# Kernel optimization log

Measured on AMD Instinct MI355X. Metric: run time of the kernel, lower is better.

The kernel has to match this reference:

```python
import jax, jax.numpy as jnp
import numpy as np

N, E, D, H, A, L = 100000, 600000, 128, 4, 32, 2
C = D // H  # per-head channels


def setup_inputs() -> dict:
    key = jax.random.key(0)
    ks = jax.random.split(key, 16)
    s = 1.0 / np.sqrt(D)
    return {
        "x": jax.random.normal(ks[0], (N, D), jnp.float32),
        "edge_index": jax.random.randint(ks[1], (2, E), 0, N, jnp.int32),
        "edge_attr": jax.random.normal(ks[2], (E, A), jnp.float32),
        # GATv2 params per layer (lin_l: source, lin_r: target, lin_edge: no bias)
        "W_l": jax.random.normal(ks[3], (L, D, D), jnp.float32) * s,
        "b_l": jnp.zeros((L, D), jnp.float32),
        "W_r": jax.random.normal(ks[4], (L, D, D), jnp.float32) * s,
        "b_r": jnp.zeros((L, D), jnp.float32),
        "W_e": jax.random.normal(ks[5], (L, A, D), jnp.float32) * (1.0 / np.sqrt(A)),
        "att": jax.random.normal(ks[6], (L, H, C), jnp.float32) * (1.0 / np.sqrt(C)),
        "bias_out": jnp.zeros((L, D), jnp.float32),
        # residual MLP: Linear -> LayerNorm -> GELU
        "lin_W": jax.random.normal(ks[7], (L, D, D), jnp.float32) * s,
        "lin_b": jnp.zeros((L, D), jnp.float32),
        "ln_gamma": jnp.ones((L, D), jnp.float32),
        "ln_beta": jnp.zeros((L, D), jnp.float32),
    }


def _gatv2_layer(x, src, dst, edge_attr, W_l, b_l, W_r, b_r, W_e, att, bias_out):
    xl = (x @ W_l + b_l).reshape(N, H, C)  # source transform
    xr = (x @ W_r + b_r).reshape(N, H, C)  # target transform
    ea = (edge_attr @ W_e).reshape(E, H, C)
    # GATv2 attention: leaky_relu(x_i + x_j + e), score with att vector
    m = jax.nn.leaky_relu(xl[src] + xr[dst] + ea, negative_slope=0.2)  # [E,H,C]
    logits = jnp.einsum('ehc,hc->eh', m, att)  # [E,H]
    # segment softmax over destination nodes
    mx = jax.ops.segment_max(logits, dst, num_segments=N)  # [N,H]
    ex = jnp.exp(logits - mx[dst])
    denom = jax.ops.segment_sum(ex, dst, num_segments=N)
    alpha = ex / denom[dst]  # [E,H]
    out = jax.ops.segment_sum(xl[src] * alpha[:, :, None], dst, num_segments=N)
    return out.reshape(N, D) + bias_out


def _mlp(h, W, b, gamma, beta):
    h = h @ W + b
    mu = jnp.mean(h, axis=-1, keepdims=True)
    var = jnp.var(h, axis=-1, keepdims=True)
    h = (h - mu) * jax.lax.rsqrt(var + 1e-5) * gamma + beta
    return jax.nn.gelu(h, approximate=False)


def reference(x, edge_index, edge_attr, W_l, b_l, W_r, b_r, W_e, att, bias_out,
              lin_W, lin_b, ln_gamma, ln_beta):
    src, dst = edge_index[0], edge_index[1]
    for i in range(L):
        x_o = _gatv2_layer(x, src, dst, edge_attr,
                           W_l[i], b_l[i], W_r[i], b_r[i], W_e[i], att[i], bias_out[i])
        x_o = _mlp(x_o, lin_W[i], lin_b[i], ln_gamma[i], ln_beta[i])
        x = x + x_o
    return x
```

## Files before the change

### kernel.cpp

```cpp
#include <hip/hip_runtime.h>
#include <cmath>

#define NN 100000
#define EE 600000
#define DD 128
#define HH 4
#define AA 32
#define CC 32
#define LL 2
#define NB ((NN + 255) / 256)
#define GEMM_GRID ((NN + 127) / 128)

typedef unsigned short u16;
typedef unsigned int u32;
typedef __attribute__((ext_vector_type(8))) short bf16x8;
typedef __attribute__((ext_vector_type(4))) float f32x4;

#define MFMA(a, b, c) __builtin_amdgcn_mfma_f32_16x16x32_bf16(a, b, c, 0, 0, 0)

__global__ __launch_bounds__(256) void k_count(const int* __restrict__ ei,
                                               int* __restrict__ cnt) {
  int e = blockIdx.x * 256 + threadIdx.x;
  if (e < EE) atomicAdd(&cnt[ei[EE + e]], 1);
}

__global__ __launch_bounds__(256) void k_scan1(const int* __restrict__ cnt,
                                               int* __restrict__ row_ptr,
                                               int* __restrict__ bsum) {
  __shared__ int buf[256];
  int b = blockIdx.x, t = threadIdx.x;
  int i = b * 256 + t;
  int v = (i < NN) ? cnt[i] : 0;
  buf[t] = v;
  __syncthreads();
  for (int off = 1; off < 256; off <<= 1) {
    int u = (t >= off) ? buf[t - off] : 0;
    __syncthreads();
    buf[t] += u;
    __syncthreads();
  }
  if (i < NN) row_ptr[i] = buf[t] - v;
  if (t == 255) bsum[b] = buf[255];
}

__global__ __launch_bounds__(512) void k_scan2(const int* __restrict__ bsum,
                                               int* __restrict__ boff) {
  __shared__ int buf[512];
  int t = threadIdx.x;
  int v = (t < NB) ? bsum[t] : 0;
  buf[t] = v;
  __syncthreads();
  for (int off = 1; off < 512; off <<= 1) {
    int u = (t >= off) ? buf[t - off] : 0;
    __syncthreads();
    buf[t] += u;
    __syncthreads();
  }
  if (t < NB) boff[t] = buf[t] - v;
}

__global__ __launch_bounds__(256) void k_scan3(int* __restrict__ row_ptr,
                                               const int* __restrict__ boff,
                                               int* __restrict__ cursor) {
  int b = blockIdx.x, t = threadIdx.x;
  int i = b * 256 + t;
  if (i < NN) {
    int v = row_ptr[i] + boff[b];
    row_ptr[i] = v;
    cursor[i] = v;
  }
  if (i == 0) row_ptr[NN] = EE;
}

__global__ __launch_bounds__(256) void k_fill(const int* __restrict__ ei,
                                              int* __restrict__ cursor,
                                              int* __restrict__ csr_e,
                                              int* __restrict__ csr_src) {
  int e = blockIdx.x * 256 + threadIdx.x;
  if (e < EE) {
    int d = ei[EE + e];
    int p = atomicAdd(&cursor[d], 1);
    csr_e[p] = e;
    csr_src[p] = ei[e];
  }
}

__global__ __launch_bounds__(256) void k_wprep(const float* __restrict__ Wl,
                                               const float* __restrict__ Wr,
                                               const float* __restrict__ Wlin,
                                               u16* __restrict__ wth,
                                               u16* __restrict__ wtl) {
  int b = blockIdx.x;
  int m = b >> 6;
  int layer = m / 3, type = m % 3;
  const float* src =
      (type == 0 ? Wl : type == 1 ? Wr : Wlin) + (size_t)layer * DD * DD;
  u16* dh = wth + (size_t)m * DD * DD;
  u16* dl = wtl + (size_t)m * DD * DD;
  int i = (b & 63) * 256 + threadIdx.x;
  int k = i >> 7, n = i & 127;
  float x = src[i];
  u32 u = __float_as_uint(x);
  u32 hr = (u + 0x7FFFu + ((u >> 16) & 1u)) & 0xFFFF0000u;
  float hf = __uint_as_float(hr);
  float d = x - hf;
  u32 u2 = __float_as_uint(d);
  u32 lr = (u2 + 0x7FFFu + ((u2 >> 16) & 1u)) & 0xFFFF0000u;
  dh[n * DD + k] = (u16)(hr >> 16);
  dl[n * DD + k] = (u16)(lr >> 16);
}

__device__ inline void cvt8(const float4& p0, const float4& p1, bf16x8& hi,
                            bf16x8& lo) {
  union { bf16x8 v; u32 u[4]; } H, L;
  float f[8] = {p0.x, p0.y, p0.z, p0.w, p1.x, p1.y, p1.z, p1.w};
#pragma unroll
  for (int i = 0; i < 4; ++i) {
    u32 u0 = __float_as_uint(f[2 * i]), u1 = __float_as_uint(f[2 * i + 1]);
    u32 h0 = u0 & 0xFFFF0000u, h1 = u1 & 0xFFFF0000u;
    H.u[i] = (h0 >> 16) | h1;
    float r0 = f[2 * i] - __uint_as_float(h0);
    float r1 = f[2 * i + 1] - __uint_as_float(h1);
    u32 l0 = __float_as_uint(r0) & 0xFFFF0000u;
    u32 l1 = __float_as_uint(r1) & 0xFFFF0000u;
    L.u[i] = (l0 >> 16) | l1;
  }
  hi = H.v;
  lo = L.v;
}

__device__ inline void load_a(const float* __restrict__ X, long row0, int wid,
                              int q, int ln, bf16x8 ah[2][4], bf16x8 al[2][4]) {
#pragma unroll
  for (int mt = 0; mt < 2; ++mt) {
    long r = row0 + wid * 32 + mt * 16 + ln;
    if (r > NN - 1) r = NN - 1;
    const float* xp = X + r * DD;
#pragma unroll
    for (int ks = 0; ks < 4; ++ks) {
      float4 p0 = *(const float4*)&xp[ks * 32 + q * 8];
      float4 p1 = *(const float4*)&xp[ks * 32 + q * 8 + 4];
      cvt8(p0, p1, ah[mt][ks], al[mt][ks]);
    }
  }
}

__device__ inline void stage_w(const u16* __restrict__ gWh,
                               const u16* __restrict__ gWl, u16* sWh, u16* sWl,
                               int t) {
  const uint4* gh = (const uint4*)gWh;
  const uint4* gl = (const uint4*)gWl;
#pragma unroll
  for (int i = 0; i < 8; ++i) {
    int c = t + 256 * i;
    int row = c >> 4;
    int bo = (c & 15) * 16;
    int dst = row * 256 + (bo ^ ((row & 7) << 4));
    *(uint4*)((char*)sWh + dst) = gh[c];
    *(uint4*)((char*)sWl + dst) = gl[c];
  }
}

__device__ inline void mfma_compute(const u16* sWh, const u16* sWl,
                                    bf16x8 ah[2][4], bf16x8 al[2][4],
                                    f32x4 acc[2][8], int q, int ln) {
#pragma unroll
  for (int ks = 0; ks < 4; ++ks) {
    int base = ks * 64 + q * 16;
#pragma unroll
    for (int nt = 0; nt < 8; ++nt) {
      int nrow = nt * 16 + ln;
      int off = nrow * 256 + (base ^ ((nrow & 7) << 4));
      bf16x8 bh = *(const bf16x8*)((const char*)sWh + off);
      bf16x8 bl = *(const bf16x8*)((const char*)sWl + off);
#pragma unroll
      for (int mt = 0; mt < 2; ++mt) {
        acc[mt][nt] = MFMA(ah[mt][ks], bh, acc[mt][nt]);
        acc[mt][nt] = MFMA(al[mt][ks], bh, acc[mt][nt]);
        acc[mt][nt] = MFMA(ah[mt][ks], bl, acc[mt][nt]);
      }
    }
  }
}

__global__ __launch_bounds__(256, 2) void k_gemm2(
    const float* __restrict__ X, const u16* __restrict__ Wh0,
    const u16* __restrict__ Wl0, const float* __restrict__ b0,
    const u16* __restrict__ Wh1, const u16* __restrict__ Wl1,
    const float* __restrict__ b1, float* __restrict__ O0,
    float* __restrict__ O1) {
  __shared__ u16 sWh[DD * DD];
  __shared__ u16 sWl[DD * DD];
  int t = threadIdx.x, wid = t >> 6, lane = t & 63;
  int q = lane >> 4, ln = lane & 15;
  long row0 = (long)blockIdx.x * 128;

  bf16x8 ah[2][4], al[2][4];
  load_a(X, row0, wid, q, ln, ah, al);

#pragma unroll 1
  for (int rep = 0; rep < 2; ++rep) {
    if (rep) __syncthreads();
    stage_w(rep ? Wh1 : Wh0, rep ? Wl1 : Wl0, sWh, sWl, t);
    __syncthreads();

    f32x4 acc[2][8];
    f32x4 zero = {0.f, 0.f, 0.f, 0.f};
#pragma unroll
    for (int mt = 0; mt < 2; ++mt)
#pragma unroll
      for (int nt = 0; nt < 8; ++nt) acc[mt][nt] = zero;

    mfma_compute(sWh, sWl, ah, al, acc, q, ln);

    const float* bias = rep ? b1 : b0;
    float* Out = rep ? O1 : O0;
    float bv[8];
#pragma unroll
    for (int nt = 0; nt < 8; ++nt) bv[nt] = bias[nt * 16 + ln];
#pragma unroll
    for (int mt = 0; mt < 2; ++mt)
#pragma unroll
      for (int nt = 0; nt < 8; ++nt)
#pragma unroll
        for (int rg = 0; rg < 4; ++rg) {
          long r = row0 + wid * 32 + mt * 16 + 4 * q + rg;
          if (r < NN) Out[r * DD + nt * 16 + ln] = acc[mt][nt][rg] + bv[nt];
        }
  }
}

__global__ __launch_bounds__(256, 2) void k_gemm_epi(
    const float* __restrict__ X, const u16* __restrict__ Wh,
    const u16* __restrict__ Wl, const float* __restrict__ bias,
    float* __restrict__ Out, const float* __restrict__ gamma,
    const float* __restrict__ beta) {
  __shared__ u16 sWh[DD * DD];
  __shared__ u16 sWl[DD * DD];
  int t = threadIdx.x, wid = t >> 6, lane = t & 63;
  int q = lane >> 4, ln = lane & 15;
  long row0 = (long)blockIdx.x * 128;

  bf16x8 ah[2][4], al[2][4];
  load_a(X, row0, wid, q, ln, ah, al);
  stage_w(Wh, Wl, sWh, sWl, t);
  __syncthreads();

  f32x4 acc[2][8];
  f32x4 zero = {0.f, 0.f, 0.f, 0.f};
#pragma unroll
  for (int mt = 0; mt < 2; ++mt)
#pragma unroll
    for (int nt = 0; nt < 8; ++nt) acc[mt][nt] = zero;

  mfma_compute(sWh, sWl, ah, al, acc, q, ln);

  float bv[8], gv[8], bev[8];
#pragma unroll
  for (int nt = 0; nt < 8; ++nt) {
    int c = nt * 16 + ln;
    bv[nt] = bias[c];
    gv[nt] = gamma[c];
    bev[nt] = beta[c];
  }

#pragma unroll
  for (int mt = 0; mt < 2; ++mt) {
    float s[4] = {0.f, 0.f, 0.f, 0.f}, ss[4] = {0.f, 0.f, 0.f, 0.f};
#pragma unroll
    for (int nt = 0; nt < 8; ++nt)
#pragma unroll
      for (int rg = 0; rg < 4; ++rg) {
        float v = acc[mt][nt][rg] + bv[nt];
        acc[mt][nt][rg] = v;
        s[rg] += v;
        ss[rg] += v * v;
      }
#pragma unroll
    for (int rg = 0; rg < 4; ++rg) {
#pragma unroll
      for (int m = 1; m < 16; m <<= 1) {
        s[rg] += __shfl_xor(s[rg], m);
        ss[rg] += __shfl_xor(ss[rg], m);
      }
    }
    float mean[4], inv[4];
#pragma unroll
    for (int rg = 0; rg < 4; ++rg) {
      mean[rg] = s[rg] * (1.f / DD);
      float var = ss[rg] * (1.f / DD) - mean[rg] * mean[rg];
      inv[rg] = rsqrtf(var + 1e-5f);
    }
    const float is2 = 0.70710678118654752440f;
#pragma unroll
    for (int nt = 0; nt < 8; ++nt)
#pragma unroll
      for (int rg = 0; rg < 4; ++rg) {
        long r = row0 + wid * 32 + mt * 16 + 4 * q + rg;
        if (r < NN) {
          int c = nt * 16 + ln;
          float u = (acc[mt][nt][rg] - mean[rg]) * inv[rg] * gv[nt] + bev[nt];
          float res = Out[r * DD + c];
          Out[r * DD + c] = res + 0.5f * u * (1.f + erff(u * is2));
        }
      }
  }
}

__global__ __launch_bounds__(256) void k_attn(const int* __restrict__ row_ptr,
                                              const int* __restrict__ csr_e,
                                              const int* __restrict__ csr_src,
                                              const float* __restrict__ eattr,
                                              const float* __restrict__ We,
                                              const float* __restrict__ att,
                                              const float* __restrict__ xl,
                                              const float* __restrict__ xr,
                                              const float* __restrict__ bias_out,
                                              float* __restrict__ xo) {
  int t = threadIdx.x;
  int wid = t >> 6, l = t & 63;
  int n = blockIdx.x * 4 + wid;
  int ch = 2 * l;

  float2 wreg[32];
#pragma unroll
  for (int a = 0; a < 32; ++a) wreg[a] = *(const float2*)&We[a * DD + ch];
  float2 av = *(const float2*)&att[ch];
  float2 xrv = *(const float2*)&xr[(size_t)n * DD + ch];

  float m = -INFINITY, d = 0.f;
  float ax = 0.f, ay = 0.f;

  int b = row_ptr[n], e2 = row_ptr[n + 1];
#pragma unroll 1
  for (int j = b; j < e2; ++j) {
    int e = __builtin_amdgcn_readfirstlane(csr_e[j]);
    int s = __builtin_amdgcn_readfirstlane(csr_src[j]);

    float eax = 0.f, eay = 0.f;
    const float4* ev = (const float4*)(eattr + (size_t)e * AA);
#pragma unroll
    for (int qq = 0; qq < 8; ++qq) {
      float4 v = ev[qq];
      float2 w0 = wreg[4 * qq + 0], w1 = wreg[4 * qq + 1];
      float2 w2 = wreg[4 * qq + 2], w3 = wreg[4 * qq + 3];
      eax = fmaf(v.x, w0.x, fmaf(v.y, w1.x, fmaf(v.z, w2.x, fmaf(v.w, w3.x, eax))));
      eay = fmaf(v.x, w0.y, fmaf(v.y, w1.y, fmaf(v.z, w2.y, fmaf(v.w, w3.y, eay))));
    }
    float2 xlv = *(const float2*)&xl[(size_t)s * DD + ch];
    float mx = xlv.x + xrv.x + eax;
    float my = xlv.y + xrv.y + eay;
    mx = mx > 0.f ? mx : 0.2f * mx;
    my = my > 0.f ? my : 0.2f * my;
    float lg = av.x * mx + av.y * my;
    lg += __shfl_xor(lg, 1);
    lg += __shfl_xor(lg, 2);
    lg += __shfl_xor(lg, 4);
    lg += __shfl_xor(lg, 8);

    float mn = fmaxf(m, lg);
    float sc = __expf(m - mn);
    float w = __expf(lg - mn);
    d = d * sc + w;
    ax = fmaf(ax, sc, w * xlv.x);
    ay = fmaf(ay, sc, w * xlv.y);
    m = mn;
  }

  float inv = d > 0.f ? 1.f / d : 0.f;
  float2 bo = *(const float2*)&bias_out[ch];
  float2 o = {fmaf(ax, inv, bo.x), fmaf(ay, inv, bo.y)};
  *(float2*)&xo[(size_t)n * DD + ch] = o;
}

extern "C" void kernel_launch(void* const* d_in, const int* in_sizes, int n_in,
                              void* d_out, int out_size, void* d_ws,
                              size_t ws_size, hipStream_t stream) {
  const float* x_in = (const float*)d_in[0];
  const int* ei = (const int*)d_in[1];
  const float* eattr = (const float*)d_in[2];
  const float* W_l = (const float*)d_in[3];
  const float* b_l = (const float*)d_in[4];
  const float* W_r = (const float*)d_in[5];
  const float* b_r = (const float*)d_in[6];
  const float* W_e = (const float*)d_in[7];
  const float* att = (const float*)d_in[8];
  const float* bias_out = (const float*)d_in[9];
  const float* lin_W = (const float*)d_in[10];
  const float* lin_b = (const float*)d_in[11];
  const float* ln_g = (const float*)d_in[12];
  const float* ln_b2 = (const float*)d_in[13];

  float* x = (float*)d_out;

  char* base = (char*)d_ws;
  size_t off = 0;
  auto alloc = [&](size_t bytes) {
    size_t o = off;
    off = (off + bytes + 255) & ~(size_t)255;
    return o;
  };
  float* xl = (float*)(base + alloc((size_t)NN * DD * 4));
  float* xr = (float*)(base + alloc((size_t)NN * DD * 4));
  float* xo = (float*)(base + alloc((size_t)NN * DD * 4));
  int* cnt = (int*)(base + alloc((size_t)NN * 4));
  int* row_ptr = (int*)(base + alloc((size_t)(NN + 1) * 4));
  int* cursor = (int*)(base + alloc((size_t)NN * 4));
  int* bsum = (int*)(base + alloc((size_t)NB * 4));
  int* boff = (int*)(base + alloc((size_t)NB * 4));
  int* csr_e = (int*)(base + alloc((size_t)EE * 4));
  int* csr_src = (int*)(base + alloc((size_t)EE * 4));
  u16* wth = (u16*)(base + alloc((size_t)6 * DD * DD * 2));
  u16* wtl = (u16*)(base + alloc((size_t)6 * DD * DD * 2));

  hipMemcpyAsync(x, x_in, (size_t)NN * DD * 4, hipMemcpyDeviceToDevice, stream);

  k_wprep<<<6 * 64, 256, 0, stream>>>(W_l, W_r, lin_W, wth, wtl);

  hipMemsetAsync(cnt, 0, (size_t)NN * 4, stream);
  k_count<<<(EE + 255) / 256, 256, 0, stream>>>(ei, cnt);
  k_scan1<<<NB, 256, 0, stream>>>(cnt, row_ptr, bsum);
  k_scan2<<<1, 512, 0, stream>>>(bsum, boff);
  k_scan3<<<NB, 256, 0, stream>>>(row_ptr, boff, cursor);
  k_fill<<<(EE + 255) / 256, 256, 0, stream>>>(ei, cursor, csr_e, csr_src);

  for (int i = 0; i < LL; ++i) {
    const u16* h_l = wth + (size_t)(i * 3 + 0) * DD * DD;
    const u16* l_l = wtl + (size_t)(i * 3 + 0) * DD * DD;
    const u16* h_r = wth + (size_t)(i * 3 + 1) * DD * DD;
    const u16* l_r = wtl + (size_t)(i * 3 + 1) * DD * DD;
    const u16* h_e = wth + (size_t)(i * 3 + 2) * DD * DD;
    const u16* l_e = wtl + (size_t)(i * 3 + 2) * DD * DD;
    const float* bl_i = b_l + (size_t)i * DD;
    const float* br_i = b_r + (size_t)i * DD;
    const float* We_i = W_e + (size_t)i * AA * DD;
    const float* att_i = att + (size_t)i * HH * CC;
    const float* bo_i = bias_out + (size_t)i * DD;
    const float* lb_i = lin_b + (size_t)i * DD;
    const float* g_i = ln_g + (size_t)i * DD;
    const float* be_i = ln_b2 + (size_t)i * DD;

    k_gemm2<<<GEMM_GRID, 256, 0, stream>>>(x, h_l, l_l, bl_i, h_r, l_r, br_i,
                                           xl, xr);
    k_attn<<<NN / 4, 256, 0, stream>>>(row_ptr, csr_e, csr_src, eattr, We_i,
                                       att_i, xl, xr, bo_i, xo);
    k_gemm_epi<<<GEMM_GRID, 256, 0, stream>>>(xo, h_e, l_e, lb_i, x, g_i, be_i);
  }
}
```

Before: 898.0 us.

## Permute edge attributes into CSR order and prefetch source rows in attention

The fill kernel now copies each edge's attribute row into destination-sorted CSR order, so the attention kernel streams edge attributes contiguously instead of gathering them through csr_e. The attention loop software-prefetches xl rows two edges ahead, sets a launch-bounds occupancy hint, and splits the edge-feature dot product into explicit FMA chains. The initial device-to-device copy of x is dropped by reading the input directly in layer 0 and passing a separate residual pointer to the epilogue GEMM. The cost is an extra 77 MB permuted attribute buffer written once, in exchange for fewer scattered reads across the two layers.

```diff
diff --git a/kernel.cpp b/kernel.cpp
--- a/kernel.cpp
+++ b/kernel.cpp
@@ -74,14 +74,18 @@
 
 __global__ __launch_bounds__(256) void k_fill(const int* __restrict__ ei,
                                               int* __restrict__ cursor,
-                                              int* __restrict__ csr_e,
-                                              int* __restrict__ csr_src) {
+                                              int* __restrict__ csr_src,
+                                              float* __restrict__ ea_perm,
+                                              const float* __restrict__ eattr) {
   int e = blockIdx.x * 256 + threadIdx.x;
   if (e < EE) {
     int d = ei[EE + e];
     int p = atomicAdd(&cursor[d], 1);
-    csr_e[p] = e;
     csr_src[p] = ei[e];
+    const float4* srow = (const float4*)(eattr + (size_t)e * AA);
+    float4* drow = (float4*)(ea_perm + (size_t)p * AA);
+#pragma unroll
+    for (int i = 0; i < 8; ++i) drow[i] = srow[i];
   }
 }
 
@@ -233,8 +237,8 @@
 __global__ __launch_bounds__(256, 2) void k_gemm_epi(
     const float* __restrict__ X, const u16* __restrict__ Wh,
     const u16* __restrict__ Wl, const float* __restrict__ bias,
-    float* __restrict__ Out, const float* __restrict__ gamma,
-    const float* __restrict__ beta) {
+    const float* __restrict__ resid, float* __restrict__ Out,
+    const float* __restrict__ gamma, const float* __restrict__ beta) {
   __shared__ u16 sWh[DD * DD];
   __shared__ u16 sWl[DD * DD];
   int t = threadIdx.x, wid = t >> 6, lane = t & 63;
@@ -300,23 +304,19 @@
         if (r < NN) {
           int c = nt * 16 + ln;
           float u = (acc[mt][nt][rg] - mean[rg]) * inv[rg] * gv[nt] + bev[nt];
-          float res = Out[r * DD + c];
+          float res = resid[r * DD + c];
           Out[r * DD + c] = res + 0.5f * u * (1.f + erff(u * is2));
         }
       }
   }
 }
 
-__global__ __launch_bounds__(256) void k_attn(const int* __restrict__ row_ptr,
-                                              const int* __restrict__ csr_e,
-                                              const int* __restrict__ csr_src,
-                                              const float* __restrict__ eattr,
-                                              const float* __restrict__ We,
-                                              const float* __restrict__ att,
-                                              const float* __restrict__ xl,
-                                              const float* __restrict__ xr,
-                                              const float* __restrict__ bias_out,
-                                              float* __restrict__ xo) {
+__global__ __launch_bounds__(256, 4) void k_attn(
+    const int* __restrict__ row_ptr, const int* __restrict__ csr_src,
+    const float* __restrict__ ea, const float* __restrict__ We,
+    const float* __restrict__ att, const float* __restrict__ xl,
+    const float* __restrict__ xr, const float* __restrict__ bias_out,
+    float* __restrict__ xo) {
   int t = threadIdx.x;
   int wid = t >> 6, l = t & 63;
   int n = blockIdx.x * 4 + wid;
@@ -332,39 +332,67 @@
   float ax = 0.f, ay = 0.f;
 
   int b = row_ptr[n], e2 = row_ptr[n + 1];
+  if (b < e2) {
+    int last = e2 - 1;
+    int s0 = csr_src[b];
+    float2 x0 = *(const float2*)&xl[(size_t)s0 * DD + ch];
+    int j1 = (b + 1 <= last) ? b + 1 : last;
+    int s1 = csr_src[j1];
+    float2 x1 = *(const float2*)&xl[(size_t)s1 * DD + ch];
+
 #pragma unroll 1
-  for (int j = b; j < e2; ++j) {
-    int e = __builtin_amdgcn_readfirstlane(csr_e[j]);
-    int s = __builtin_amdgcn_readfirstlane(csr_src[j]);
-
-    float eax = 0.f, eay = 0.f;
-    const float4* ev = (const float4*)(eattr + (size_t)e * AA);
-#pragma unroll
-    for (int qq = 0; qq < 8; ++qq) {
-      float4 v = ev[qq];
-      float2 w0 = wreg[4 * qq + 0], w1 = wreg[4 * qq + 1];
-      float2 w2 = wreg[4 * qq + 2], w3 = wreg[4 * qq + 3];
-      eax = fmaf(v.x, w0.x, fmaf(v.y, w1.x, fmaf(v.z, w2.x, fmaf(v.w, w3.x, eax))));
-      eay = fmaf(v.x, w0.y, fmaf(v.y, w1.y, fmaf(v.z, w2.y, fmaf(v.w, w3.y, eay))));
+    for (int j = b; j < e2; ++j) {
+      const float4* ev = (const float4*)(ea + (size_t)j * AA);
+      float4 v0 = ev[0], v1 = ev[1], v2 = ev[2], v3 = ev[3];
+      float4 v4 = ev[4], v5 = ev[5], v6 = ev[6], v7 = ev[7];
+
+      float2 cxl = x0;
+      x0 = x1;
+      int j2 = (j + 2 <= last) ? j + 2 : last;
+      int s2 = csr_src[j2];
+      x1 = *(const float2*)&xl[(size_t)s2 * DD + ch];
+
+      float eax, eay;
+      {
+        float ex0, ey0;
+        ex0 = fmaf(v0.x, wreg[0].x, fmaf(v0.y, wreg[1].x, fmaf(v0.z, wreg[2].x, v0.w * wreg[3].x)));
+        ey0 = fmaf(v0.x, wreg[0].y, fmaf(v0.y, wreg[1].y, fmaf(v0.z, wreg[2].y, v0.w * wreg[3].y)));
+        ex0 = fmaf(v1.x, wreg[4].x, fmaf(v1.y, wreg[5].x, fmaf(v1.z, wreg[6].x, fmaf(v1.w, wreg[7].x, ex0))));
+        ey0 = fmaf(v1.x, wreg[4].y, fmaf(v1.y, wreg[5].y, fmaf(v1.z, wreg[6].y, fmaf(v1.w, wreg[7].y, ey0))));
+        ex0 = fmaf(v2.x, wreg[8].x, fmaf(v2.y, wreg[9].x, fmaf(v2.z, wreg[10].x, fmaf(v2.w, wreg[11].x, ex0))));
+        ey0 = fmaf(v2.x, wreg[8].y, fmaf(v2.y, wreg[9].y, fmaf(v2.z, wreg[10].y, fmaf(v2.w, wreg[11].y, ey0))));
+        ex0 = fmaf(v3.x, wreg[12].x, fmaf(v3.y, wreg[13].x, fmaf(v3.z, wreg[14].x, fmaf(v3.w, wreg[15].x, ex0))));
+        ey0 = fmaf(v3.x, wreg[12].y, fmaf(v3.y, wreg[13].y, fmaf(v3.z, wreg[14].y, fmaf(v3.w, wreg[15].y, ey0))));
+        ex0 = fmaf(v4.x, wreg[16].x, fmaf(v4.y, wreg[17].x, fmaf(v4.z, wreg[18].x, fmaf(v4.w, wreg[19].x, ex0))));
+        ey0 = fmaf(v4.x, wreg[16].y, fmaf(v4.y, wreg[17].y, fmaf(v4.z, wreg[18].y, fmaf(v4.w, wreg[19].y, ey0))));
+        ex0 = fmaf(v5.x, wreg[20].x, fmaf(v5.y, wreg[21].x, fmaf(v5.z, wreg[22].x, fmaf(v5.w, wreg[23].x, ex0))));
+        ey0 = fmaf(v5.x, wreg[20].y, fmaf(v5.y, wreg[21].y, fmaf(v5.z, wreg[22].y, fmaf(v5.w, wreg[23].y, ey0))));
+        ex0 = fmaf(v6.x, wreg[24].x, fmaf(v6.y, wreg[25].x, fmaf(v6.z, wreg[26].x, fmaf(v6.w, wreg[27].x, ex0))));
+        ey0 = fmaf(v6.x, wreg[24].y, fmaf(v6.y, wreg[25].y, fmaf(v6.z, wreg[26].y, fmaf(v6.w, wreg[27].y, ey0))));
+        ex0 = fmaf(v7.x, wreg[28].x, fmaf(v7.y, wreg[29].x, fmaf(v7.z, wreg[30].x, fmaf(v7.w, wreg[31].x, ex0))));
+        ey0 = fmaf(v7.x, wreg[28].y, fmaf(v7.y, wreg[29].y, fmaf(v7.z, wreg[30].y, fmaf(v7.w, wreg[31].y, ey0))));
+        eax = ex0;
+        eay = ey0;
+      }
+
+      float mx = cxl.x + xrv.x + eax;
+      float my = cxl.y + xrv.y + eay;
+      mx = mx > 0.f ? mx : 0.2f * mx;
+      my = my > 0.f ? my : 0.2f * my;
+      float lg = av.x * mx + av.y * my;
+      lg += __shfl_xor(lg, 1);
+      lg += __shfl_xor(lg, 2);
+      lg += __shfl_xor(lg, 4);
+      lg += __shfl_xor(lg, 8);
+
+      float mn = fmaxf(m, lg);
+      float sc = __expf(m - mn);
+      float w = __expf(lg - mn);
+      d = d * sc + w;
+      ax = fmaf(ax, sc, w * cxl.x);
+      ay = fmaf(ay, sc, w * cxl.y);
+      m = mn;
     }
-    float2 xlv = *(const float2*)&xl[(size_t)s * DD + ch];
-    float mx = xlv.x + xrv.x + eax;
-    float my = xlv.y + xrv.y + eay;
-    mx = mx > 0.f ? mx : 0.2f * mx;
-    my = my > 0.f ? my : 0.2f * my;
-    float lg = av.x * mx + av.y * my;
-    lg += __shfl_xor(lg, 1);
-    lg += __shfl_xor(lg, 2);
-    lg += __shfl_xor(lg, 4);
-    lg += __shfl_xor(lg, 8);
-
-    float mn = fmaxf(m, lg);
-    float sc = __expf(m - mn);
-    float w = __expf(lg - mn);
-    d = d * sc + w;
-    ax = fmaf(ax, sc, w * xlv.x);
-    ay = fmaf(ay, sc, w * xlv.y);
-    m = mn;
   }
 
   float inv = d > 0.f ? 1.f / d : 0.f;
@@ -403,17 +431,15 @@
   float* xl = (float*)(base + alloc((size_t)NN * DD * 4));
   float* xr = (float*)(base + alloc((size_t)NN * DD * 4));
   float* xo = (float*)(base + alloc((size_t)NN * DD * 4));
+  float* ea_perm = (float*)(base + alloc((size_t)EE * AA * 4));
   int* cnt = (int*)(base + alloc((size_t)NN * 4));
   int* row_ptr = (int*)(base + alloc((size_t)(NN + 1) * 4));
   int* cursor = (int*)(base + alloc((size_t)NN * 4));
   int* bsum = (int*)(base + alloc((size_t)NB * 4));
   int* boff = (int*)(base + alloc((size_t)NB * 4));
-  int* csr_e = (int*)(base + alloc((size_t)EE * 4));
   int* csr_src = (int*)(base + alloc((size_t)EE * 4));
   u16* wth = (u16*)(base + alloc((size_t)6 * DD * DD * 2));
   u16* wtl = (u16*)(base + alloc((size_t)6 * DD * DD * 2));
-
-  hipMemcpyAsync(x, x_in, (size_t)NN * DD * 4, hipMemcpyDeviceToDevice, stream);
 
   k_wprep<<<6 * 64, 256, 0, stream>>>(W_l, W_r, lin_W, wth, wtl);
 
@@ -422,7 +448,8 @@
   k_scan1<<<NB, 256, 0, stream>>>(cnt, row_ptr, bsum);
   k_scan2<<<1, 512, 0, stream>>>(bsum, boff);
   k_scan3<<<NB, 256, 0, stream>>>(row_ptr, boff, cursor);
-  k_fill<<<(EE + 255) / 256, 256, 0, stream>>>(ei, cursor, csr_e, csr_src);
+  k_fill<<<(EE + 255) / 256, 256, 0, stream>>>(ei, cursor, csr_src, ea_perm,
+                                               eattr);
 
   for (int i = 0; i < LL; ++i) {
     const u16* h_l = wth + (size_t)(i * 3 + 0) * DD * DD;
@@ -440,10 +467,13 @@
     const float* g_i = ln_g + (size_t)i * DD;
     const float* be_i = ln_b2 + (size_t)i * DD;
 
-    k_gemm2<<<GEMM_GRID, 256, 0, stream>>>(x, h_l, l_l, bl_i, h_r, l_r, br_i,
-                                           xl, xr);
-    k_attn<<<NN / 4, 256, 0, stream>>>(row_ptr, csr_e, csr_src, eattr, We_i,
-                                       att_i, xl, xr, bo_i, xo);
-    k_gemm_epi<<<GEMM_GRID, 256, 0, stream>>>(xo, h_e, l_e, lb_i, x, g_i, be_i);
-  }
-}
+    const float* xcur = (i == 0) ? x_in : x;
+
+    k_gemm2<<<GEMM_GRID, 256, 0, stream>>>(xcur, h_l, l_l, bl_i, h_r, l_r,
+                                           br_i, xl, xr);
+    k_attn<<<NN / 4, 256, 0, stream>>>(row_ptr, csr_src, ea_perm, We_i, att_i,
+                                       xl, xr, bo_i, xo);
+    k_gemm_epi<<<GEMM_GRID, 256, 0, stream>>>(xo, h_e, l_e, lb_i, xcur, x, g_i,
+                                              be_i);
+  }
+}
```

Measured after the change: 1.327 ms. +47.7%, slower.
